# Kernel optimization log

Measured on AMD Instinct MI355X. Metric: run time of the kernel, lower is better.

The kernel has to match this reference:

```python
import jax, jax.numpy as jnp
import numpy as np
import math

B, R, D = 1, 2, 256
NH, NL, NP, ZA = 8, 1, 8, 4
H = W = 128
Q = H * W
HD = D // NH


def _bilinear(v, loc, Hl, Wl):
    # v: [BH, Hl*Wl, hd]; loc: [BH, Q, P, 2] normalized to [0,1]
    x = loc[..., 0] * Wl - 0.5
    y = loc[..., 1] * Hl - 0.5
    x0f = jnp.floor(x); y0f = jnp.floor(y)
    wx = (x - x0f)[..., None]; wy = (y - y0f)[..., None]
    x0 = x0f.astype(jnp.int32); y0 = y0f.astype(jnp.int32)
    def corner(iy, ix):
        valid = (iy >= 0) & (iy < Hl) & (ix >= 0) & (ix < Wl)
        idx = jnp.clip(iy, 0, Hl - 1) * Wl + jnp.clip(ix, 0, Wl - 1)
        g = jax.vmap(lambda vb, ib: vb[ib])(v, idx)  # [BH,Q,P,hd]
        return g * valid[..., None].astype(v.dtype)
    g00 = corner(y0, x0); g01 = corner(y0, x0 + 1)
    g10 = corner(y0 + 1, x0); g11 = corner(y0 + 1, x0 + 1)
    return (g00 * (1 - wx) + g01 * wx) * (1 - wy) + (g10 * (1 - wx) + g11 * wx) * wy


def setup_inputs() -> dict:
    key = jax.random.key(0)
    ks = jax.random.split(key, 12)
    query = jax.random.normal(ks[0], (B, Q, D), jnp.float32)
    value = jax.random.normal(ks[1], (B * R, Q, D), jnp.float32)
    reference_points = jax.random.uniform(ks[2], (R, Q, ZA, 2), jnp.float32)
    spatial_shapes = jnp.array([[H, W]], jnp.int32)
    # sampling_offsets: zero-ish weight + directional grid bias (as in init_weights)
    W_off = 0.01 * jax.random.normal(ks[3], (NH * NL * NP * 2, D), jnp.float32)
    thetas = jnp.arange(NH, dtype=jnp.float32) * (2.0 * math.pi / NH)
    grid = jnp.stack([jnp.cos(thetas), jnp.sin(thetas)], -1)
    grid = grid / jnp.max(jnp.abs(grid), axis=-1, keepdims=True)
    grid = jnp.tile(grid[:, None, None, :], (1, NL, NP, 1))
    grid = grid * (jnp.arange(1, NP + 1, dtype=jnp.float32)[None, None, :, None])
    b_off = grid.reshape(-1)
    W_attn = 0.01 * jax.random.normal(ks[4], (NH * NL * NP, D), jnp.float32)
    b_attn = 0.01 * jax.random.normal(ks[5], (NH * NL * NP,), jnp.float32)
    s = 1.0 / np.sqrt(D)
    W_val = s * jax.random.normal(ks[6], (D, D), jnp.float32)
    b_val = jnp.zeros((D,), jnp.float32)
    W_out = s * jax.random.normal(ks[7], (D, D), jnp.float32)
    b_out = jnp.zeros((D,), jnp.float32)
    return {"query": query, "value": value, "reference_points": reference_points,
            "spatial_shapes": spatial_shapes, "W_off": W_off, "b_off": b_off,
            "W_attn": W_attn, "b_attn": b_attn, "W_val": W_val, "b_val": b_val,
            "W_out": W_out, "b_out": b_out}


def reference(query, value, reference_points, spatial_shapes,
              W_off, b_off, W_attn, b_attn, W_val, b_val, W_out, b_out):
    shapes = np.asarray(spatial_shapes)  # static level shapes
    residual = query
    Bq, nq, d = query.shape
    Rr, _, za, _ = reference_points.shape
    # rebatch query/reference_points over histories -> batch Bq*Rr (== value batch)
    q = jnp.broadcast_to(query[:, None], (Bq, Rr, nq, d)).reshape(Bq * Rr, nq, d)
    rp = jnp.broadcast_to(reference_points[None], (Bq, Rr, nq, za, 2)).reshape(Bq * Rr, nq, za, 2)
    bs = value.shape[0]
    v = (value @ W_val.T + b_val).reshape(bs, -1, NH, HD)
    off = (q @ W_off.T + b_off).reshape(bs, nq, NH, NL, NP, 2)
    aw = jax.nn.softmax((q @ W_attn.T + b_attn).reshape(bs, nq, NH, NL * NP), axis=-1)
    aw = aw.reshape(bs, nq, NH, NL, NP)
    norm = jnp.stack([shapes[:, 1].astype(np.float32), shapes[:, 0].astype(np.float32)], -1)  # [NL,2] = (W,H)
    off = off / norm[None, None, None, :, None, :]
    off = off.reshape(bs, nq, NH, NL, NP // za, za, 2)
    loc = rp[:, :, None, None, None, :, :] + off  # [bs,nq,NH,NL,NP//za,za,2]
    loc = loc.reshape(bs, nq, NH, NL, NP, 2)
    # multi-scale deformable attention (gather + bilinear + weighted sum)
    starts = np.concatenate([[0], np.cumsum(shapes[:, 0] * shapes[:, 1])])
    out = jnp.zeros((bs * NH, nq, HD), v.dtype)
    for l in range(NL):
        Hl, Wl = int(shapes[l, 0]), int(shapes[l, 1])
        vl = v[:, starts[l]:starts[l + 1]].transpose(0, 2, 1, 3).reshape(bs * NH, Hl * Wl, HD)
        locl = loc[:, :, :, l].transpose(0, 2, 1, 3, 4).reshape(bs * NH, nq, NP, 2)
        sampled = _bilinear(vl, locl, Hl, Wl)  # [bs*NH, nq, NP, hd]
        awl = aw[:, :, :, l].transpose(0, 2, 1, 3).reshape(bs * NH, nq, NP)
        out = out + jnp.einsum('bqph,bqp->bqh', sampled, awl)
    out = out.reshape(bs, NH, nq, HD).transpose(0, 2, 1, 3).reshape(bs, nq, d)
    out = out.mean(0, keepdims=True)  # mean over history-batch dim -> [1,nq,d]
    out = out @ W_out.T + b_out
    return out + residual  # dropout is identity in eval
```

## Files before the change

### kernel.cpp

```cpp
#include <hip/hip_runtime.h>
#include <hip/hip_bf16.h>
#include <hip/hip_fp16.h>

#define QN 16384
#define DK 256

typedef float f4_t __attribute__((ext_vector_type(4)));
typedef short s16x8 __attribute__((ext_vector_type(8)));
typedef short s16x4 __attribute__((ext_vector_type(4)));
typedef unsigned int u32;
typedef u32 u32x4 __attribute__((ext_vector_type(4)));
typedef __fp16 h2_t __attribute__((ext_vector_type(2)));

__device__ inline short f2bf(float f){
  __hip_bfloat16 h = __float2bfloat16(f);
  return __builtin_bit_cast(short, h);
}
__device__ inline short f2h16(float f){
  __half h = __float2half(f);
  return __builtin_bit_cast(short, h);
}
__device__ inline float dot2h(u32 a, u32 b, float c){
#if __has_builtin(__builtin_amdgcn_fdot2)
  return __builtin_amdgcn_fdot2(__builtin_bit_cast(h2_t, a),
                                __builtin_bit_cast(h2_t, b), c, false);
#else
  h2_t ha = __builtin_bit_cast(h2_t, a), hb = __builtin_bit_cast(h2_t, b);
  return c + (float)ha[0] * (float)hb[0] + (float)ha[1] * (float)hb[1];
#endif
}
__device__ inline u32 pk2h(float a, float b){
#if __has_builtin(__builtin_amdgcn_cvt_pkrtz)
  h2_t r = __builtin_amdgcn_cvt_pkrtz(a, b);
  return __builtin_bit_cast(u32, r);
#else
  return (u32)__builtin_bit_cast(unsigned short, __float2half(a)) |
         ((u32)__builtin_bit_cast(unsigned short, __float2half(b)) << 16);
#endif
}
__device__ inline u32 bperm(u32 s0, u32 s1, u32 sel){
  return __builtin_amdgcn_perm(s0, s1, sel);
}

__global__ __launch_bounds__(256) void k_convw(const float* __restrict__ Wv,
    const float* __restrict__ Woff, const float* __restrict__ Wattn,
    const float* __restrict__ Wout, short* __restrict__ Wbf){
  const int base = (blockIdx.x * 256 + threadIdx.x) * 16;
  #pragma unroll
  for (int c = 0; c < 4; ++c){
    const int e = base + c * 4;
    const int row = e >> 8, col = e & 255;
    const float* src;
    int r = row;
    if (row < 256)       src = Wv    + (size_t)r * DK;
    else if (row < 384){ src = Woff  + (size_t)(r - 256) * DK; }
    else if (row < 448){ src = Wattn + (size_t)(r - 384) * DK; }
    else               { src = Wout  + (size_t)(r - 448) * DK; }
    const f4_t v = *(const f4_t*)(src + col);
    s16x4 o = { f2bf(v[0]), f2bf(v[1]), f2bf(v[2]), f2bf(v[3]) };
    *(s16x4*)(Wbf + e) = o;
  }
}

__global__ __launch_bounds__(256, 2) void k_proj(const float* __restrict__ value,
    const float* __restrict__ query, const short* __restrict__ Wbf,
    const float* __restrict__ bval, const float* __restrict__ boff,
    const float* __restrict__ battn, short* __restrict__ vhf,
    float* __restrict__ offw, float* __restrict__ logit){
  __shared__ short As[64 * 256];
  __shared__ short Bs[64 * 256];
  const int tid = threadIdx.x;
  const int lane = tid & 63, wv = tid >> 6;
  const int r16 = lane & 15, kh = lane >> 4;
  const int swsel = (r16 & 7) << 4;
  const int bid = blockIdx.x;

  if (bid < 512){
    const float* A = value;
    const short* Bw = Wbf;
    const int mbase = bid * 64;
    #pragma unroll
    for (int i = 0; i < 16; ++i){
      const int lin = i * 256 + tid;
      const int r = lin >> 6, ck = lin & 63;
      const f4_t v = *(const f4_t*)(A + (size_t)(mbase + r) * DK + ck * 4);
      s16x4 o = { f2bf(v[0]), f2bf(v[1]), f2bf(v[2]), f2bf(v[3]) };
      *(s16x4*)((char*)As + r * 512 + ((ck * 8) ^ ((r & 7) << 4))) = o;
    }
    s16x8 breg[8];
    #pragma unroll
    for (int i = 0; i < 8; ++i){
      const int lin = i * 256 + tid;
      const int n = lin >> 5, ck = lin & 31;
      breg[i] = *(const s16x8*)(Bw + (size_t)n * DK + ck * 8);
    }
    __syncthreads();
    for (int cg = 0; cg < 4; ++cg){
      #pragma unroll
      for (int i = 0; i < 8; ++i){
        const int lin = i * 256 + tid;
        const int n = lin >> 5, ck = lin & 31;
        *(s16x8*)((char*)Bs + n * 512 + ((ck * 16) ^ ((n & 7) << 4))) = breg[i];
      }
      __syncthreads();
      if (cg < 3){
        #pragma unroll
        for (int i = 0; i < 8; ++i){
          const int lin = i * 256 + tid;
          const int n = lin >> 5, ck = lin & 31;
          breg[i] = *(const s16x8*)(Bw + (size_t)((cg + 1) * 64 + n) * DK + ck * 8);
        }
      }
      f4_t acc[4];
      #pragma unroll
      for (int i = 0; i < 4; ++i) acc[i] = (f4_t){0.f, 0.f, 0.f, 0.f};
      #pragma unroll
      for (int kk = 0; kk < 8; ++kk){
        const int kb = kh * 16 + kk * 64;
        const s16x8 a = *(const s16x8*)((char*)As + (wv * 16 + r16) * 512 + (kb ^ swsel));
        #pragma unroll
        for (int nt = 0; nt < 4; ++nt){
          const s16x8 b = *(const s16x8*)((char*)Bs + (nt * 16 + r16) * 512 + (kb ^ swsel));
          acc[nt] = __builtin_amdgcn_mfma_f32_16x16x32_bf16(a, b, acc[nt], 0, 0, 0);
        }
      }
      #pragma unroll
      for (int nt = 0; nt < 4; ++nt){
        const int n = cg * 64 + nt * 16 + r16;
        const int h = n >> 5, hd = n & 31;
        const float bv = bval[n];
        #pragma unroll
        for (int rix = 0; rix < 4; ++rix){
          const int m = mbase + wv * 16 + kh * 4 + rix;
          const int r = m >> 14, pix = m & (QN - 1);
          vhf[(size_t)((r * 8 + h) * QN + pix) * 32 + hd] = f2h16(acc[nt][rix] + bv);
        }
      }
      __syncthreads();
    }
  } else {
    const float* A = query;
    const short* Bw = Wbf + 256 * DK;
    const int mg = wv & 1, ch = wv >> 1;
    const int mbase = (bid - 512) * 32;
    #pragma unroll
    for (int i = 0; i < 8; ++i){
      const int lin = i * 256 + tid;
      const int r = lin >> 6, ck = lin & 63;
      const f4_t v = *(const f4_t*)(A + (size_t)(mbase + r) * DK + ck * 4);
      s16x4 o = { f2bf(v[0]), f2bf(v[1]), f2bf(v[2]), f2bf(v[3]) };
      *(s16x4*)((char*)As + r * 512 + ((ck * 8) ^ ((r & 7) << 4))) = o;
    }
    s16x8 breg[8];
    #pragma unroll
    for (int i = 0; i < 8; ++i){
      const int lin = i * 256 + tid;
      const int n = lin >> 5, ck = lin & 31;
      breg[i] = *(const s16x8*)(Bw + (size_t)n * DK + ck * 8);
    }
    __syncthreads();
    for (int cg = 0; cg < 3; ++cg){
      #pragma unroll
      for (int i = 0; i < 8; ++i){
        const int lin = i * 256 + tid;
        const int n = lin >> 5, ck = lin & 31;
        *(s16x8*)((char*)Bs + n * 512 + ((ck * 16) ^ ((n & 7) << 4))) = breg[i];
      }
      __syncthreads();
      if (cg < 2){
        #pragma unroll
        for (int i = 0; i < 8; ++i){
          const int lin = i * 256 + tid;
          const int n = lin >> 5, ck = lin & 31;
          breg[i] = *(const s16x8*)(Bw + (size_t)((cg + 1) * 64 + n) * DK + ck * 8);
        }
      }
      f4_t acc[2];
      acc[0] = (f4_t){0.f,0.f,0.f,0.f}; acc[1] = (f4_t){0.f,0.f,0.f,0.f};
      #pragma unroll
      for (int kk = 0; kk < 8; ++kk){
        const int kb = kh * 16 + kk * 64;
        const s16x8 a = *(const s16x8*)((char*)As + (mg * 16 + r16) * 512 + (kb ^ swsel));
        #pragma unroll
        for (int nt = 0; nt < 2; ++nt){
          const s16x8 b = *(const s16x8*)((char*)Bs + (ch * 32 + nt * 16 + r16) * 512 + (kb ^ swsel));
          acc[nt] = __builtin_amdgcn_mfma_f32_16x16x32_bf16(a, b, acc[nt], 0, 0, 0);
        }
      }
      #pragma unroll
      for (int nt = 0; nt < 2; ++nt){
        const int n = cg * 64 + ch * 32 + nt * 16 + r16;
        #pragma unroll
        for (int rix = 0; rix < 4; ++rix){
          const int m = mbase + mg * 16 + kh * 4 + rix;
          const float v = acc[nt][rix];
          if (n < 128) offw[(size_t)m * 128 + n] = v + boff[n];
          else         logit[(size_t)m * 64 + (n - 128)] = v + battn[n - 128];
        }
      }
      __syncthreads();
    }
  }
}

__global__ __launch_bounds__(256, 2) void k_gemm_out(const short* __restrict__ Ab,
    const short* __restrict__ Bw, const float* __restrict__ bout,
    const float* __restrict__ query, float* __restrict__ out){
  __shared__ short As[32 * 256];
  __shared__ short Bs[64 * 256];
  const int tid = threadIdx.x;
  const int lane = tid & 63, wv = tid >> 6;
  const int r16 = lane & 15, kh = lane >> 4;
  const int mg = wv & 1, ch = wv >> 1;
  const int swsel = (r16 & 7) << 4;
  const int mbase = blockIdx.x * 32;

  #pragma unroll
  for (int i = 0; i < 4; ++i){
    const int lin = i * 256 + tid;
    const int r = lin >> 5, ck = lin & 31;
    const s16x8 v = *(const s16x8*)(Ab + (size_t)(mbase + r) * DK + ck * 8);
    *(s16x8*)((char*)As + r * 512 + ((ck * 16) ^ ((r & 7) << 4))) = v;
  }
  s16x8 breg[8];
  #pragma unroll
  for (int i = 0; i < 8; ++i){
    const int lin = i * 256 + tid;
    const int n = lin >> 5, ck = lin & 31;
    breg[i] = *(const s16x8*)(Bw + (size_t)n * DK + ck * 8);
  }
  __syncthreads();

  for (int cg = 0; cg < 4; ++cg){
    #pragma unroll
    for (int i = 0; i < 8; ++i){
      const int lin = i * 256 + tid;
      const int n = lin >> 5, ck = lin & 31;
      *(s16x8*)((char*)Bs + n * 512 + ((ck * 16) ^ ((n & 7) << 4))) = breg[i];
    }
    __syncthreads();
    if (cg < 3){
      #pragma unroll
      for (int i = 0; i < 8; ++i){
        const int lin = i * 256 + tid;
        const int n = lin >> 5, ck = lin & 31;
        breg[i] = *(const s16x8*)(Bw + (size_t)((cg + 1) * 64 + n) * DK + ck * 8);
      }
    }
    f4_t acc[2];
    acc[0] = (f4_t){0.f,0.f,0.f,0.f}; acc[1] = (f4_t){0.f,0.f,0.f,0.f};
    #pragma unroll
    for (int kk = 0; kk < 8; ++kk){
      const int kb = kh * 16 + kk * 64;
      const s16x8 a = *(const s16x8*)((char*)As + (mg * 16 + r16) * 512 + (kb ^ swsel));
      #pragma unroll
      for (int nt = 0; nt < 2; ++nt){
        const s16x8 b = *(const s16x8*)((char*)Bs + (ch * 32 + nt * 16 + r16) * 512 + (kb ^ swsel));
        acc[nt] = __builtin_amdgcn_mfma_f32_16x16x32_bf16(a, b, acc[nt], 0, 0, 0);
      }
    }
    #pragma unroll
    for (int nt = 0; nt < 2; ++nt){
      const int n = cg * 64 + ch * 32 + nt * 16 + r16;
      const float bo = bout[n];
      #pragma unroll
      for (int rix = 0; rix < 4; ++rix){
        const int m = mbase + mg * 16 + kh * 4 + rix;
        out[(size_t)m * DK + n] = acc[nt][rix] + bo + query[(size_t)m * DK + n];
      }
    }
    __syncthreads();
  }
}

__device__ inline void mkw(float rx, float ry, float ox, float oy, float awp,
                           u32& word, u32& pk01, u32& pk23){
  const float x = fmaf(rx, 128.f, ox) - 0.5f;
  const float y = fmaf(ry, 128.f, oy) - 0.5f;
  const float xf = floorf(x), yf = floorf(y);
  const float wx = x - xf, wy = y - yf;
  const int ix = (int)xf, iy = (int)yf;
  float xw0 = 1.f - wx, xw1 = wx, yw0 = 1.f - wy, yw1 = wy;
  if (ix < 0 || ix > 127)   xw0 = 0.f;
  if (ix < -1 || ix > 126)  xw1 = 0.f;
  if (iy < 0 || iy > 127)   yw0 = 0.f;
  if (iy < -1 || iy > 126)  yw1 = 0.f;
  const int ix0 = min(max(ix, 0), 127), ix1 = min(max(ix + 1, 0), 127);
  const int iy0 = min(max(iy, 0), 127), iy1 = min(max(iy + 1, 0), 127);
  const float t0 = awp * yw0, t1 = awp * yw1;
  pk01 = pk2h(t0 * xw0, t0 * xw1);
  pk23 = pk2h(t1 * xw0, t1 * xw1);
  word = (u32)(iy0 * 128 + ix0) | ((u32)(ix1 - ix0) << 16) | ((u32)(iy1 - iy0) << 17);
}

__global__ __launch_bounds__(256) void k_sampler(const float* __restrict__ rp,
    const float* __restrict__ offw, const float* __restrict__ logit,
    const short* __restrict__ vhf, short* __restrict__ O2b){
  const int tid = threadIdx.x;
  const int j3 = tid & 7;
  const int cj = j3 & 3;
  const int px = j3 >> 2;
  const int grp = tid >> 3;
  const int lane = tid & 63;
  const int glane8 = lane & ~7;
  const int h = blockIdx.x & 7;
  const int q = (blockIdx.x >> 3) * 32 + grp;
  const u32 cjof = (u32)cj * 8;
  const u32 selw = px ? 0x03020706u : 0x01000504u;

  const float* lp = logit + (size_t)q * 64 + h * 8;
  const float l = lp[j3];
  float m = l;
  m = fmaxf(m, __shfl_xor(m, 1)); m = fmaxf(m, __shfl_xor(m, 2)); m = fmaxf(m, __shfl_xor(m, 4));
  const float e = __expf(l - m);
  float ssum = e;
  ssum += __shfl_xor(ssum, 1); ssum += __shfl_xor(ssum, 2); ssum += __shfl_xor(ssum, 4);
  const float awp = e * (0.5f / ssum);

  const float* offp = offw + (size_t)q * 128 + h * 16;
  const float ox = offp[2 * j3], oy = offp[2 * j3 + 1];
  const int za2 = (j3 & 3) * 2;
  const float rx0 = rp[(size_t)q * 8 + za2],        ry0 = rp[(size_t)q * 8 + za2 + 1];
  const float rx1 = rp[(size_t)(QN + q) * 8 + za2], ry1 = rp[(size_t)(QN + q) * 8 + za2 + 1];

  u32 wrdA, pkA01, pkA23, wrdB, pkB01, pkB23;
  mkw(rx0, ry0, ox, oy, awp, wrdA, pkA01, pkA23);
  mkw(rx1, ry1, ox, oy, awp, wrdB, pkB01, pkB23);

  const short* vb0 = vhf + (size_t)(h * QN) * 32;
  const short* vb1 = vhf + (size_t)((8 + h) * QN) * 32;

  float acc[8] = {0.f,0.f,0.f,0.f,0.f,0.f,0.f,0.f};

#define LOADP(S, WRD, VB)                                                   \
  const u32 wd_##S = __shfl((WRD), glane8 | ((S) & 7));                     \
  const u32 o0_##S = (wd_##S & 0xFFFFu) * 32u + cjof                        \
                   + (px ? ((wd_##S >> 11) & 32u) : 0u);                    \
  const u32 o1_##S = o0_##S + ((wd_##S >> 17) & 1u) * 4096u;                \
  const u32x4 cA_##S = *(const u32x4*)((VB) + o0_##S);                      \
  const u32x4 cB_##S = *(const u32x4*)((VB) + o1_##S);

#define USEP(S, PK01, PK23) do{                                             \
    const int srcl_ = glane8 | ((S) & 7);                                   \
    const u32 w01_ = __shfl((PK01), srcl_);                                 \
    const u32 w23_ = __shfl((PK23), srcl_);                                 \
    const u32 wp_  = bperm(w01_, w23_, selw);                               \
    _Pragma("unroll")                                                       \
    for (int e_ = 0; e_ < 4; ++e_){                                         \
      const u32 pl_ = bperm(cA_##S[e_], cB_##S[e_], 0x01000504u);           \
      const u32 ph_ = bperm(cA_##S[e_], cB_##S[e_], 0x03020706u);           \
      acc[2*e_]   = dot2h(pl_, wp_, acc[2*e_]);                             \
      acc[2*e_+1] = dot2h(ph_, wp_, acc[2*e_+1]);                           \
    }                                                                       \
  }while(0)

  LOADP(0,  wrdA, vb0) LOADP(1,  wrdA, vb0) LOADP(2,  wrdA, vb0)
  USEP(0,  pkA01, pkA23); LOADP(3,  wrdA, vb0)
  USEP(1,  pkA01, pkA23); LOADP(4,  wrdA, vb0)
  USEP(2,  pkA01, pkA23); LOADP(5,  wrdA, vb0)
  USEP(3,  pkA01, pkA23); LOADP(6,  wrdA, vb0)
  USEP(4,  pkA01, pkA23); LOADP(7,  wrdA, vb0)
  USEP(5,  pkA01, pkA23); LOADP(8,  wrdB, vb1)
  USEP(6,  pkA01, pkA23); LOADP(9,  wrdB, vb1)
  USEP(7,  pkA01, pkA23); LOADP(10, wrdB, vb1)
  USEP(8,  pkB01, pkB23); LOADP(11, wrdB, vb1)
  USEP(9,  pkB01, pkB23); LOADP(12, wrdB, vb1)
  USEP(10, pkB01, pkB23); LOADP(13, wrdB, vb1)
  USEP(11, pkB01, pkB23); LOADP(14, wrdB, vb1)
  USEP(12, pkB01, pkB23); LOADP(15, wrdB, vb1)
  USEP(13, pkB01, pkB23);
  USEP(14, pkB01, pkB23);
  USEP(15, pkB01, pkB23);
#undef LOADP
#undef USEP

  #pragma unroll
  for (int i = 0; i < 8; ++i) acc[i] += __shfl_xor(acc[i], 4);
  if (px == 0){
    s16x8 o = { f2bf(acc[0]), f2bf(acc[1]), f2bf(acc[2]), f2bf(acc[3]),
                f2bf(acc[4]), f2bf(acc[5]), f2bf(acc[6]), f2bf(acc[7]) };
    *(s16x8*)(O2b + (size_t)q * DK + h * 32 + cj * 8) = o;
  }
}

extern "C" void kernel_launch(void* const* d_in, const int* in_sizes, int n_in,
                              void* d_out, int out_size, void* d_ws, size_t ws_size,
                              hipStream_t stream) {
  const float* query = (const float*)d_in[0];
  const float* value = (const float*)d_in[1];
  const float* refpt = (const float*)d_in[2];
  const float* W_off  = (const float*)d_in[4];
  const float* b_off  = (const float*)d_in[5];
  const float* W_attn = (const float*)d_in[6];
  const float* b_attn = (const float*)d_in[7];
  const float* W_val  = (const float*)d_in[8];
  const float* b_val  = (const float*)d_in[9];
  const float* W_out  = (const float*)d_in[10];
  const float* b_out  = (const float*)d_in[11];
  float* out = (float*)d_out;

  char* ws = (char*)d_ws;
  short* Wbf  = (short*)(ws);
  short* vhf  = (short*)(ws + 360448);
  float* offw = (float*)(ws + 17137664);
  float* logit= (float*)(ws + 25526272);
  short* O2b  = (short*)(ws + 29720576);

  k_convw   <<<dim3(44),   dim3(256), 0, stream>>>(W_val, W_off, W_attn, W_out, Wbf);
  k_proj    <<<dim3(1024), dim3(256), 0, stream>>>(value, query, Wbf, b_val, b_off,
                                                   b_attn, vhf, offw, logit);
  k_sampler <<<dim3(4096), dim3(256), 0, stream>>>(refpt, offw, logit, vhf, O2b);
  k_gemm_out<<<dim3(512),  dim3(256), 0, stream>>>(O2b, Wbf + 448 * DK, b_out, query, out);
}
```

Before: 71.88 us.

## Store projected values as FP8 and gather FP8 in the sampler

The value projection now writes its output in FP8 e4m3 instead of FP16. The result is staged through shared memory so each thread issues one 16-byte coalesced store rather than scattered 2-byte stores. The sampler gathers half as many bytes per corner and unpacks them with cvt_pk_f32_fp8, accumulating with FP32 FMAs. This halves value storage and gather traffic, at the cost of FP8 quantization error, which may exceed the accuracy tolerance, plus extra unpack instructions.

New measurement: 67.84 us. -5.6%, faster.

```diff
diff --git a/kernel.cpp b/kernel.cpp
--- a/kernel.cpp
+++ b/kernel.cpp
@@ -1,33 +1,23 @@
 #include <hip/hip_runtime.h>
 #include <hip/hip_bf16.h>
 #include <hip/hip_fp16.h>
+#include <hip/hip_fp8.h>
 
 #define QN 16384
 #define DK 256
 
 typedef float f4_t __attribute__((ext_vector_type(4)));
+typedef float f2_t __attribute__((ext_vector_type(2)));
 typedef short s16x8 __attribute__((ext_vector_type(8)));
 typedef short s16x4 __attribute__((ext_vector_type(4)));
 typedef unsigned int u32;
 typedef u32 u32x4 __attribute__((ext_vector_type(4)));
+typedef u32 u32x2 __attribute__((ext_vector_type(2)));
 typedef __fp16 h2_t __attribute__((ext_vector_type(2)));
 
 __device__ inline short f2bf(float f){
   __hip_bfloat16 h = __float2bfloat16(f);
   return __builtin_bit_cast(short, h);
-}
-__device__ inline short f2h16(float f){
-  __half h = __float2half(f);
-  return __builtin_bit_cast(short, h);
-}
-__device__ inline float dot2h(u32 a, u32 b, float c){
-#if __has_builtin(__builtin_amdgcn_fdot2)
-  return __builtin_amdgcn_fdot2(__builtin_bit_cast(h2_t, a),
-                                __builtin_bit_cast(h2_t, b), c, false);
-#else
-  h2_t ha = __builtin_bit_cast(h2_t, a), hb = __builtin_bit_cast(h2_t, b);
-  return c + (float)ha[0] * (float)hb[0] + (float)ha[1] * (float)hb[1];
-#endif
 }
 __device__ inline u32 pk2h(float a, float b){
 #if __has_builtin(__builtin_amdgcn_cvt_pkrtz)
@@ -40,6 +30,26 @@
 }
 __device__ inline u32 bperm(u32 s0, u32 s1, u32 sel){
   return __builtin_amdgcn_perm(s0, s1, sel);
+}
+__device__ inline u32 pk_fp8(float a, float b){
+#if __has_builtin(__builtin_amdgcn_cvt_pk_fp8_f32)
+  return (u32)__builtin_amdgcn_cvt_pk_fp8_f32(a, b, 0, false);
+#else
+  __hip_fp8_e4m3 fa(a), fb(b);
+  return (u32)fa.__x | ((u32)fb.__x << 8);
+#endif
+}
+template<bool HI>
+__device__ inline f2_t upk_fp8(u32 w){
+#if __has_builtin(__builtin_amdgcn_cvt_pk_f32_fp8)
+  return __builtin_amdgcn_cvt_pk_f32_fp8(w, HI);
+#else
+  const u32 hh = HI ? (w >> 16) : (w & 0xFFFFu);
+  __hip_fp8_e4m3 a, b;
+  a.__x = (unsigned char)(hh & 0xFF);
+  b.__x = (unsigned char)(hh >> 8);
+  return (f2_t){(float)a, (float)b};
+#endif
 }
 
 __global__ __launch_bounds__(256) void k_convw(const float* __restrict__ Wv,
@@ -51,11 +61,10 @@
     const int e = base + c * 4;
     const int row = e >> 8, col = e & 255;
     const float* src;
-    int r = row;
-    if (row < 256)       src = Wv    + (size_t)r * DK;
-    else if (row < 384){ src = Woff  + (size_t)(r - 256) * DK; }
-    else if (row < 448){ src = Wattn + (size_t)(r - 384) * DK; }
-    else               { src = Wout  + (size_t)(r - 448) * DK; }
+    if (row < 256)       src = Wv    + (size_t)row * DK;
+    else if (row < 384)  src = Woff  + (size_t)(row - 256) * DK;
+    else if (row < 448)  src = Wattn + (size_t)(row - 384) * DK;
+    else                 src = Wout  + (size_t)(row - 448) * DK;
     const f4_t v = *(const f4_t*)(src + col);
     s16x4 o = { f2bf(v[0]), f2bf(v[1]), f2bf(v[2]), f2bf(v[3]) };
     *(s16x4*)(Wbf + e) = o;
@@ -65,10 +74,11 @@
 __global__ __launch_bounds__(256, 2) void k_proj(const float* __restrict__ value,
     const float* __restrict__ query, const short* __restrict__ Wbf,
     const float* __restrict__ bval, const float* __restrict__ boff,
-    const float* __restrict__ battn, short* __restrict__ vhf,
+    const float* __restrict__ battn, char* __restrict__ vfp8,
     float* __restrict__ offw, float* __restrict__ logit){
   __shared__ short As[64 * 256];
   __shared__ short Bs[64 * 256];
+  __shared__ u32 Cs[64 * 16];
   const int tid = threadIdx.x;
   const int lane = tid & 63, wv = tid >> 6;
   const int r16 = lane & 15, kh = lane >> 4;
@@ -127,16 +137,23 @@
       #pragma unroll
       for (int nt = 0; nt < 4; ++nt){
         const int n = cg * 64 + nt * 16 + r16;
-        const int h = n >> 5, hd = n & 31;
         const float bv = bval[n];
         #pragma unroll
         for (int rix = 0; rix < 4; ++rix){
-          const int m = mbase + wv * 16 + kh * 4 + rix;
-          const int r = m >> 14, pix = m & (QN - 1);
-          vhf[(size_t)((r * 8 + h) * QN + pix) * 32 + hd] = f2h16(acc[nt][rix] + bv);
+          const float vv = acc[nt][rix] + bv;
+          ((char*)Cs)[(wv * 16 + kh * 4 + rix) * 64 + nt * 16 + r16] =
+              (char)(pk_fp8(vv, 0.f) & 0xFFu);
         }
       }
       __syncthreads();
+      {
+        const u32x4 cw = *((const u32x4*)((const char*)Cs + tid * 16));
+        const int pixl = tid >> 2, q4 = tid & 3;
+        const int h2 = cg * 2 + (q4 >> 1);
+        const int m = mbase + pixl;
+        const int r = m >> 14, pix = m & (QN - 1);
+        *(u32x4*)(vfp8 + ((size_t)((r * 8 + h2) * QN + pix)) * 32 + (q4 & 1) * 16) = cw;
+      }
     }
   } else {
     const float* A = query;
@@ -295,7 +312,7 @@
 
 __global__ __launch_bounds__(256) void k_sampler(const float* __restrict__ rp,
     const float* __restrict__ offw, const float* __restrict__ logit,
-    const short* __restrict__ vhf, short* __restrict__ O2b){
+    const char* __restrict__ vfp8, short* __restrict__ O2b){
   const int tid = threadIdx.x;
   const int j3 = tid & 7;
   const int cj = j3 & 3;
@@ -327,8 +344,8 @@
   mkw(rx0, ry0, ox, oy, awp, wrdA, pkA01, pkA23);
   mkw(rx1, ry1, ox, oy, awp, wrdB, pkB01, pkB23);
 
-  const short* vb0 = vhf + (size_t)(h * QN) * 32;
-  const short* vb1 = vhf + (size_t)((8 + h) * QN) * 32;
+  const char* vb0 = vfp8 + (size_t)(h * QN) * 32;
+  const char* vb1 = vfp8 + (size_t)((8 + h) * QN) * 32;
 
   float acc[8] = {0.f,0.f,0.f,0.f,0.f,0.f,0.f,0.f};
 
@@ -337,20 +354,25 @@
   const u32 o0_##S = (wd_##S & 0xFFFFu) * 32u + cjof                        \
                    + (px ? ((wd_##S >> 11) & 32u) : 0u);                    \
   const u32 o1_##S = o0_##S + ((wd_##S >> 17) & 1u) * 4096u;                \
-  const u32x4 cA_##S = *(const u32x4*)((VB) + o0_##S);                      \
-  const u32x4 cB_##S = *(const u32x4*)((VB) + o1_##S);
+  const u32x2 cA_##S = *(const u32x2*)((VB) + o0_##S);    \
+  const u32x2 cB_##S = *(const u32x2*)((VB) + o1_##S);
 
 #define USEP(S, PK01, PK23) do{                                             \
     const int srcl_ = glane8 | ((S) & 7);                                   \
     const u32 w01_ = __shfl((PK01), srcl_);                                 \
     const u32 w23_ = __shfl((PK23), srcl_);                                 \
-    const u32 wp_  = bperm(w01_, w23_, selw);                               \
+    const h2_t wp_ = __builtin_bit_cast(h2_t, bperm(w01_, w23_, selw));     \
+    const float w0_ = (float)wp_[0], w1_ = (float)wp_[1];                   \
     _Pragma("unroll")                                                       \
-    for (int e_ = 0; e_ < 4; ++e_){                                         \
-      const u32 pl_ = bperm(cA_##S[e_], cB_##S[e_], 0x01000504u);           \
-      const u32 ph_ = bperm(cA_##S[e_], cB_##S[e_], 0x03020706u);           \
-      acc[2*e_]   = dot2h(pl_, wp_, acc[2*e_]);                             \
-      acc[2*e_+1] = dot2h(ph_, wp_, acc[2*e_+1]);                           \
+    for (int wdi_ = 0; wdi_ < 2; ++wdi_){                                   \
+      const f2_t aL_ = upk_fp8<false>(cA_##S[wdi_]);                        \
+      const f2_t aH_ = upk_fp8<true >(cA_##S[wdi_]);                        \
+      const f2_t bL_ = upk_fp8<false>(cB_##S[wdi_]);                        \
+      const f2_t bH_ = upk_fp8<true >(cB_##S[wdi_]);                        \
+      acc[4*wdi_+0] = fmaf(w0_, aL_[0], fmaf(w1_, bL_[0], acc[4*wdi_+0]));  \
+      acc[4*wdi_+1] = fmaf(w0_, aL_[1], fmaf(w1_, bL_[1], acc[4*wdi_+1]));  \
+      acc[4*wdi_+2] = fmaf(w0_, aH_[0], fmaf(w1_, bH_[0], acc[4*wdi_+2]));  \
+      acc[4*wdi_+3] = fmaf(w0_, aH_[1], fmaf(w1_, bH_[1], acc[4*wdi_+3]));  \
     }                                                                       \
   }while(0)
 
@@ -401,14 +423,14 @@
 
   char* ws = (char*)d_ws;
   short* Wbf  = (short*)(ws);
-  short* vhf  = (short*)(ws + 360448);
-  float* offw = (float*)(ws + 17137664);
-  float* logit= (float*)(ws + 25526272);
-  short* O2b  = (short*)(ws + 29720576);
+  char*  vfp8 = (char*)(ws + 360448);
+  float* offw = (float*)(ws + 8749056);
+  float* logit= (float*)(ws + 17137664);
+  short* O2b  = (short*)(ws + 21331968);
 
   k_convw   <<<dim3(44),   dim3(256), 0, stream>>>(W_val, W_off, W_attn, W_out, Wbf);
   k_proj    <<<dim3(1024), dim3(256), 0, stream>>>(value, query, Wbf, b_val, b_off,
-                                                   b_attn, vhf, offw, logit);
-  k_sampler <<<dim3(4096), dim3(256), 0, stream>>>(refpt, offw, logit, vhf, O2b);
+                                                   b_attn, vfp8, offw, logit);
+  k_sampler <<<dim3(4096), dim3(256), 0, stream>>>(refpt, offw, logit, vfp8, O2b);
   k_gemm_out<<<dim3(512),  dim3(256), 0, stream>>>(O2b, Wbf + 448 * DK, b_out, query, out);
 }
```
